# Kernel optimization log

Hardware: AMD Instinct MI355X
Metric: run time of the kernel (lower is better)

Reference implementation:

```python
import jax, jax.numpy as jnp
import numpy as np
import math

N_HEADS = 8

def setup_inputs() -> dict:
    key = jax.random.key(0)
    qkv = jax.random.normal(key, (4, 1536, 2048), dtype=jnp.float32)
    return {"qkv": qkv}

def reference(qkv) -> jnp.ndarray:
    bs, width, length = qkv.shape
    ch = width // (3 * N_HEADS)
    q, k, v = jnp.split(qkv, 3, axis=1)  # each (bs, n_heads*ch, T)
    scale = 1.0 / math.sqrt(math.sqrt(ch))
    q = (q * scale).reshape(bs * N_HEADS, ch, length)
    k = (k * scale).reshape(bs * N_HEADS, ch, length)
    v = v.reshape(bs * N_HEADS, ch, length)
    # scores: (bs*heads, T, T)
    weight = jnp.einsum('bct,bcs->bts', q, k)
    weight = jax.nn.softmax(weight.astype(jnp.float32), axis=-1).astype(weight.dtype)
    a = jnp.einsum('bts,bcs->bct', weight, v)
    return a.reshape(bs, -1, length)
```

## Files before the change

kernel.cpp:

```cpp
#include <hip/hip_runtime.h>
#include <hip/hip_bf16.h>
#include <math.h>


#define T_LEN 2048
#define NH    32
#define D     64
#define QLD   2048
#define LSTR  72

using f32x4 = __attribute__((ext_vector_type(4))) float;
using s16x8 = __attribute__((ext_vector_type(8))) short;
using s16x4 = __attribute__((ext_vector_type(4))) short;
using u32x4 = __attribute__((ext_vector_type(4))) unsigned;

__device__ __forceinline__ short f2bf(float f) {
    union { float f; unsigned u; } x; x.f = f;
    unsigned r = x.u + 0x7fffu + ((x.u >> 16) & 1u);
    return (short)(r >> 16);
}

#if __has_builtin(__builtin_amdgcn_exp2f)
#define EXP2(x) __builtin_amdgcn_exp2f(x)
#else
#define EXP2(x) __expf(0.6931471805599453f * (x))
#endif

__device__ __forceinline__ unsigned pack2bf(float a, float b) {
    unsigned ua = __float_as_uint(a) + 0x8000u;
    unsigned ub = __float_as_uint(b) + 0x8000u;
    return __builtin_amdgcn_perm(ub, ua, 0x07060302u);
}

__global__ __launch_bounds__(256, 4)
void prep(const float* __restrict__ qkv, short* __restrict__ ws16)
{
    __shared__ __align__(16) short tile[64 * LSTR];
    const int tid  = threadIdx.x;
    const int t0   = blockIdx.x * 64;
    const int head = blockIdx.y;
    const int kind = blockIdx.z;
    const int b = head >> 3, h = head & 7;

    short* qt = ws16;
    short* kt = ws16 + (size_t)NH * T_LEN * D;
    short* vb = kt   + (size_t)NH * T_LEN * D;

    if (kind == 2) {
        const float* src = qkv + (size_t)(b * 1536 + 1024 + h * 64) * QLD;
        int c = tid >> 2, seg = (tid & 3) * 16;
        const float* p = src + (size_t)c * QLD + t0 + seg;
        short* dst = vb + ((size_t)head * D + c) * T_LEN + t0 + seg;
        #pragma unroll
        for (int j = 0; j < 2; ++j) {
            f32x4 a  = *(const f32x4*)(p + j * 8);
            f32x4 bb = *(const f32x4*)(p + j * 8 + 4);
            s16x8 w;
            w[0]=f2bf(a[0]);  w[1]=f2bf(a[1]);  w[2]=f2bf(a[2]);  w[3]=f2bf(a[3]);
            w[4]=f2bf(bb[0]); w[5]=f2bf(bb[1]); w[6]=f2bf(bb[2]); w[7]=f2bf(bb[3]);
            *(s16x8*)(dst + j * 8) = w;
        }
        return;
    }

    const float sc = (kind == 0) ? 0.35355339059327373f * 1.4426950408889634f
                                 : 0.35355339059327373f;
    const float* src = qkv + (size_t)(b * 1536 + kind * 512 + h * 64) * QLD;
    short* dst = (kind == 0 ? qt : kt) + ((size_t)head * T_LEN + t0) * D;

    {
        int m = tid & 15, c4 = (tid >> 4) << 2;
        const float* base = src + (size_t)c4 * QLD + t0 + 4 * m;
        f32x4 r0 = *(const f32x4*)base;
        f32x4 r1 = *(const f32x4*)(base + QLD);
        f32x4 r2 = *(const f32x4*)(base + 2 * QLD);
        f32x4 r3 = *(const f32x4*)(base + 3 * QLD);
        #pragma unroll
        for (int j = 0; j < 4; ++j) {
            s16x4 w;
            w[0]=f2bf(r0[j]*sc); w[1]=f2bf(r1[j]*sc); w[2]=f2bf(r2[j]*sc); w[3]=f2bf(r3[j]*sc);
            *(s16x4*)&tile[(4 * m + j) * LSTR + c4] = w;
        }
    }
    __syncthreads();
    {
        int row = tid >> 3;
        int off = (tid & 7) * 8;
        *(s16x8*)(dst + (size_t)row * D + off)        = *(const s16x8*)&tile[row * LSTR + off];
        *(s16x8*)(dst + (size_t)(row + 32) * D + off) = *(const s16x8*)&tile[(row + 32) * LSTR + off];
    }
}

__global__ __launch_bounds__(256, 4)
void attn(const short* __restrict__ ws16, float* __restrict__ out)
{
    __shared__ __align__(16) short ktile[64 * 64];
    __shared__ __align__(16) short vtile[64 * 64];

    const int tid  = threadIdx.x;
    const int w    = tid >> 6;
    const int lane = tid & 63;
    const int l16  = lane & 15;
    const int quad = lane >> 4;

    const int bid  = blockIdx.x;
    const int head = (bid & 7) + 8 * ((bid >> 3) & 3);
    const int t0   = (bid >> 5) * 64;

    const short* qt = ws16 + (size_t)head * T_LEN * D;
    const short* kt = ws16 + (size_t)NH * T_LEN * D + (size_t)head * T_LEN * D;
    const short* vb = ws16 + 2 * (size_t)NH * T_LEN * D + (size_t)head * D * T_LEN;
    float*       op = out  + (size_t)head * 64 * QLD;

    const short* qrow = qt + (size_t)(t0 + w * 16 + l16) * D + quad * 8;
    const s16x8 bq0 = *(const s16x8*)qrow;
    const s16x8 bq1 = *(const s16x8*)(qrow + 32);

    f32x4 o[4];
    #pragma unroll
    for (int ct = 0; ct < 4; ++ct) o[ct] = f32x4{0.f, 0.f, 0.f, 0.f};
    float l_part = 0.f;

    const int kperm = (l16 >> 2) * 8 + (l16 & 3);
    const int ksw   = (l16 & 3) | (((l16 >> 2) & 1) << 2);
    const int srow  = lane >> 3;
    const int schk  = lane & 7;

    for (int it = 0; it < T_LEN / 64; ++it) {
        const int s0 = it * 64;

        #pragma unroll
        for (int n = 0; n < 2; ++n) {
            const int rl = w * 16 + n * 8 + srow;
            const int sk = (srow & 3) | (((w * 2 + n) & 1) << 2);
            s16x8 kd = *(const s16x8*)(kt + (size_t)(s0 + rl) * D + ((schk ^ sk) << 3));
            *(s16x8*)&ktile[rl * 64 + schk * 8] = kd;
            s16x8 vd = *(const s16x8*)(vb + (size_t)rl * T_LEN + s0 + ((schk ^ srow) << 3));
            *(s16x8*)&vtile[rl * 64 + schk * 8] = vd;
        }
        __syncthreads();

        #pragma unroll
        for (int g = 0; g < 2; ++g) {
            u32x4 bp;
            #pragma unroll
            for (int sub = 0; sub < 2; ++sub) {
                const int R = g * 32 + kperm + 4 * sub;
                const int c0 = (quad ^ ksw) << 3;
                s16x8 ak0 = *(const s16x8*)&ktile[R * 64 + c0];
                s16x8 ak1 = *(const s16x8*)&ktile[R * 64 + (c0 ^ 32)];
                f32x4 acc = f32x4{0.f, 0.f, 0.f, 0.f};
                acc = __builtin_amdgcn_mfma_f32_16x16x32_bf16(ak0, bq0, acc, 0, 0, 0);
                acc = __builtin_amdgcn_mfma_f32_16x16x32_bf16(ak1, bq1, acc, 0, 0, 0);
                float p0 = EXP2(acc[0]);
                float p1 = EXP2(acc[1]);
                float p2 = EXP2(acc[2]);
                float p3 = EXP2(acc[3]);
                l_part += (p0 + p1) + (p2 + p3);
                bp[sub * 2]     = pack2bf(p0, p1);
                bp[sub * 2 + 1] = pack2bf(p2, p3);
            }
            #pragma unroll
            for (int ct = 0; ct < 4; ++ct) {
                const int r = ct * 16 + l16;
                s16x8 av = *(const s16x8*)&vtile[r * 64 + ((((g * 4 + quad) ^ (l16 & 7))) << 3)];
                o[ct] = __builtin_amdgcn_mfma_f32_16x16x32_bf16(
                    av, __builtin_bit_cast(s16x8, bp), o[ct], 0, 0, 0);
            }
        }
        __syncthreads();
    }

    float l = l_part;
    l += __shfl_xor(l, 16);
    l += __shfl_xor(l, 32);
    const float inv = 1.f / l;
    const int tq = t0 + w * 16 + l16;
    #pragma unroll
    for (int ct = 0; ct < 4; ++ct) {
        #pragma unroll
        for (int r = 0; r < 4; ++r) {
            const int c = ct * 16 + quad * 4 + r;
            op[(size_t)c * QLD + tq] = o[ct][r] * inv;
        }
    }
}

extern "C" void kernel_launch(void* const* d_in, const int* in_sizes, int n_in,
                              void* d_out, int out_size, void* d_ws, size_t ws_size,
                              hipStream_t stream) {
    const float* qkv = (const float*)d_in[0];
    float* out = (float*)d_out;
    short* ws16 = (short*)d_ws;

    prep<<<dim3(T_LEN / 64, NH, 3), dim3(256), 0, stream>>>(qkv, ws16);
    attn<<<dim3(1024), dim3(256), 0, stream>>>(ws16, out);
}
```

Before: 135.5 us.

## Process two query sub-tiles per wave to reuse K/V tiles across 128 queries

Each block now handles 128 query rows instead of 64, with each wave computing two 16-row query sub-tiles that share the same K and V fragments loaded from LDS. This halves the global K/V traffic per query and the LDS reads per MFMA. In exchange it doubles accumulator registers, lowers occupancy (launch bounds reduced to 2), and halves the grid to 512 blocks, which may underfill the 256 CUs.

Measured after the change: 156.7 us. +15.7%, slower.

```diff
diff --git a/kernel.cpp b/kernel.cpp
--- a/kernel.cpp
+++ b/kernel.cpp
@@ -91,7 +91,7 @@
     }
 }
 
-__global__ __launch_bounds__(256, 4)
+__global__ __launch_bounds__(256, 2)
 void attn(const short* __restrict__ ws16, float* __restrict__ out)
 {
     __shared__ __align__(16) short ktile[64 * 64];
@@ -105,21 +105,27 @@
 
     const int bid  = blockIdx.x;
     const int head = (bid & 7) + 8 * ((bid >> 3) & 3);
-    const int t0   = (bid >> 5) * 64;
+    const int t0   = (bid >> 5) * 128;
 
     const short* qt = ws16 + (size_t)head * T_LEN * D;
     const short* kt = ws16 + (size_t)NH * T_LEN * D + (size_t)head * T_LEN * D;
     const short* vb = ws16 + 2 * (size_t)NH * T_LEN * D + (size_t)head * D * T_LEN;
     float*       op = out  + (size_t)head * 64 * QLD;
 
-    const short* qrow = qt + (size_t)(t0 + w * 16 + l16) * D + quad * 8;
-    const s16x8 bq0 = *(const s16x8*)qrow;
-    const s16x8 bq1 = *(const s16x8*)(qrow + 32);
-
-    f32x4 o[4];
+    s16x8 bq[2][2];
     #pragma unroll
-    for (int ct = 0; ct < 4; ++ct) o[ct] = f32x4{0.f, 0.f, 0.f, 0.f};
-    float l_part = 0.f;
+    for (int nq = 0; nq < 2; ++nq) {
+        const short* qrow = qt + (size_t)(t0 + w * 32 + nq * 16 + l16) * D + quad * 8;
+        bq[nq][0] = *(const s16x8*)qrow;
+        bq[nq][1] = *(const s16x8*)(qrow + 32);
+    }
+
+    f32x4 o[2][4];
+    #pragma unroll
+    for (int nq = 0; nq < 2; ++nq)
+        #pragma unroll
+        for (int ct = 0; ct < 4; ++ct) o[nq][ct] = f32x4{0.f, 0.f, 0.f, 0.f};
+    float l_part[2] = {0.f, 0.f};
 
     const int kperm = (l16 >> 2) * 8 + (l16 & 3);
     const int ksw   = (l16 & 3) | (((l16 >> 2) & 1) << 2);
@@ -142,46 +148,55 @@
 
         #pragma unroll
         for (int g = 0; g < 2; ++g) {
-            u32x4 bp;
+            u32x4 bp[2];
             #pragma unroll
             for (int sub = 0; sub < 2; ++sub) {
                 const int R = g * 32 + kperm + 4 * sub;
                 const int c0 = (quad ^ ksw) << 3;
                 s16x8 ak0 = *(const s16x8*)&ktile[R * 64 + c0];
                 s16x8 ak1 = *(const s16x8*)&ktile[R * 64 + (c0 ^ 32)];
-                f32x4 acc = f32x4{0.f, 0.f, 0.f, 0.f};
-                acc = __builtin_amdgcn_mfma_f32_16x16x32_bf16(ak0, bq0, acc, 0, 0, 0);
-                acc = __builtin_amdgcn_mfma_f32_16x16x32_bf16(ak1, bq1, acc, 0, 0, 0);
-                float p0 = EXP2(acc[0]);
-                float p1 = EXP2(acc[1]);
-                float p2 = EXP2(acc[2]);
-                float p3 = EXP2(acc[3]);
-                l_part += (p0 + p1) + (p2 + p3);
-                bp[sub * 2]     = pack2bf(p0, p1);
-                bp[sub * 2 + 1] = pack2bf(p2, p3);
+                #pragma unroll
+                for (int nq = 0; nq < 2; ++nq) {
+                    f32x4 acc = f32x4{0.f, 0.f, 0.f, 0.f};
+                    acc = __builtin_amdgcn_mfma_f32_16x16x32_bf16(ak0, bq[nq][0], acc, 0, 0, 0);
+                    acc = __builtin_amdgcn_mfma_f32_16x16x32_bf16(ak1, bq[nq][1], acc, 0, 0, 0);
+                    float p0 = EXP2(acc[0]);
+                    float p1 = EXP2(acc[1]);
+                    float p2 = EXP2(acc[2]);
+                    float p3 = EXP2(acc[3]);
+                    l_part[nq] += (p0 + p1) + (p2 + p3);
+                    bp[nq][sub * 2]     = pack2bf(p0, p1);
+                    bp[nq][sub * 2 + 1] = pack2bf(p2, p3);
+                }
             }
             #pragma unroll
             for (int ct = 0; ct < 4; ++ct) {
                 const int r = ct * 16 + l16;
                 s16x8 av = *(const s16x8*)&vtile[r * 64 + ((((g * 4 + quad) ^ (l16 & 7))) << 3)];
-                o[ct] = __builtin_amdgcn_mfma_f32_16x16x32_bf16(
-                    av, __builtin_bit_cast(s16x8, bp), o[ct], 0, 0, 0);
+                #pragma unroll
+                for (int nq = 0; nq < 2; ++nq) {
+                    o[nq][ct] = __builtin_amdgcn_mfma_f32_16x16x32_bf16(
+                        av, __builtin_bit_cast(s16x8, bp[nq]), o[nq][ct], 0, 0, 0);
+                }
             }
         }
         __syncthreads();
     }
 
-    float l = l_part;
-    l += __shfl_xor(l, 16);
-    l += __shfl_xor(l, 32);
-    const float inv = 1.f / l;
-    const int tq = t0 + w * 16 + l16;
     #pragma unroll
-    for (int ct = 0; ct < 4; ++ct) {
-        #pragma unroll
-        for (int r = 0; r < 4; ++r) {
-            const int c = ct * 16 + quad * 4 + r;
-            op[(size_t)c * QLD + tq] = o[ct][r] * inv;
+    for (int nq = 0; nq < 2; ++nq) {
+        float l = l_part[nq];
+        l += __shfl_xor(l, 16);
+        l += __shfl_xor(l, 32);
+        const float inv = 1.f / l;
+        const int tq = t0 + w * 32 + nq * 16 + l16;
+        #pragma unroll
+        for (int ct = 0; ct < 4; ++ct) {
+            #pragma unroll
+            for (int r = 0; r < 4; ++r) {
+                const int c = ct * 16 + quad * 4 + r;
+                op[(size_t)c * QLD + tq] = o[nq][ct][r] * inv;
+            }
         }
     }
 }
@@ -194,5 +209,5 @@
     short* ws16 = (short*)d_ws;
 
     prep<<<dim3(T_LEN / 64, NH, 3), dim3(256), 0, stream>>>(qkv, ws16);
-    attn<<<dim3(1024), dim3(256), 0, stream>>>(ws16, out);
-}
+    attn<<<dim3(512), dim3(256), 0, stream>>>(ws16, out);
+}
```

## Double-buffer K/V LDS tiles and prefetch next tile during compute

Applied to the files above, without the earlier changes.

Splits the K and V shared-memory tiles into two buffers. Global loads for the next iteration are issued before the MFMA work on the current tile and written to the other buffer afterwards, leaving one barrier per iteration instead of two. The aim is to hide global-memory latency behind the QK/PV compute. In exchange it doubles LDS use to 32KB per block, which could lower occupancy, and keeps the prefetched registers live across the compute.

Measured after the change: 134.7 us. Within noise of the previous version (-0.6%).

```diff
diff --git a/kernel.cpp b/kernel.cpp
--- a/kernel.cpp
+++ b/kernel.cpp
@@ -94,8 +94,8 @@
 __global__ __launch_bounds__(256, 4)
 void attn(const short* __restrict__ ws16, float* __restrict__ out)
 {
-    __shared__ __align__(16) short ktile[64 * 64];
-    __shared__ __align__(16) short vtile[64 * 64];
+    __shared__ __align__(16) short ktile[2][64 * 64];
+    __shared__ __align__(16) short vtile[2][64 * 64];
 
     const int tid  = threadIdx.x;
     const int w    = tid >> 6;
@@ -126,19 +126,36 @@
     const int srow  = lane >> 3;
     const int schk  = lane & 7;
 
+    const int rl0 = w * 16 + srow;
+    const int rl1 = rl0 + 8;
+    const int sk0 = (srow & 3) | (((w * 2 + 0) & 1) << 2);
+    const int sk1 = (srow & 3) | (((w * 2 + 1) & 1) << 2);
+    const short* kge0 = kt + (size_t)rl0 * D + ((schk ^ sk0) << 3);
+    const short* kge1 = kt + (size_t)rl1 * D + ((schk ^ sk1) << 3);
+    const short* vge0 = vb + (size_t)rl0 * T_LEN + ((schk ^ srow) << 3);
+    const short* vge1 = vb + (size_t)rl1 * T_LEN + ((schk ^ srow) << 3);
+
+    {
+        s16x8 kd0 = *(const s16x8*)(kge0);
+        s16x8 kd1 = *(const s16x8*)(kge1);
+        s16x8 vd0 = *(const s16x8*)(vge0);
+        s16x8 vd1 = *(const s16x8*)(vge1);
+        *(s16x8*)&ktile[0][rl0 * 64 + schk * 8] = kd0;
+        *(s16x8*)&ktile[0][rl1 * 64 + schk * 8] = kd1;
+        *(s16x8*)&vtile[0][rl0 * 64 + schk * 8] = vd0;
+        *(s16x8*)&vtile[0][rl1 * 64 + schk * 8] = vd1;
+    }
+
+    #pragma unroll 2
     for (int it = 0; it < T_LEN / 64; ++it) {
-        const int s0 = it * 64;
-
-        #pragma unroll
-        for (int n = 0; n < 2; ++n) {
-            const int rl = w * 16 + n * 8 + srow;
-            const int sk = (srow & 3) | (((w * 2 + n) & 1) << 2);
-            s16x8 kd = *(const s16x8*)(kt + (size_t)(s0 + rl) * D + ((schk ^ sk) << 3));
-            *(s16x8*)&ktile[rl * 64 + schk * 8] = kd;
-            s16x8 vd = *(const s16x8*)(vb + (size_t)rl * T_LEN + s0 + ((schk ^ srow) << 3));
-            *(s16x8*)&vtile[rl * 64 + schk * 8] = vd;
-        }
+        const int cur = it & 1;
         __syncthreads();
+
+        const int s0n = (it + 1 < T_LEN / 64 ? it + 1 : it) * 64;
+        s16x8 kd0 = *(const s16x8*)(kge0 + (size_t)s0n * D);
+        s16x8 kd1 = *(const s16x8*)(kge1 + (size_t)s0n * D);
+        s16x8 vd0 = *(const s16x8*)(vge0 + s0n);
+        s16x8 vd1 = *(const s16x8*)(vge1 + s0n);
 
         #pragma unroll
         for (int g = 0; g < 2; ++g) {
@@ -147,8 +164,8 @@
             for (int sub = 0; sub < 2; ++sub) {
                 const int R = g * 32 + kperm + 4 * sub;
                 const int c0 = (quad ^ ksw) << 3;
-                s16x8 ak0 = *(const s16x8*)&ktile[R * 64 + c0];
-                s16x8 ak1 = *(const s16x8*)&ktile[R * 64 + (c0 ^ 32)];
+                s16x8 ak0 = *(const s16x8*)&ktile[cur][R * 64 + c0];
+                s16x8 ak1 = *(const s16x8*)&ktile[cur][R * 64 + (c0 ^ 32)];
                 f32x4 acc = f32x4{0.f, 0.f, 0.f, 0.f};
                 acc = __builtin_amdgcn_mfma_f32_16x16x32_bf16(ak0, bq0, acc, 0, 0, 0);
                 acc = __builtin_amdgcn_mfma_f32_16x16x32_bf16(ak1, bq1, acc, 0, 0, 0);
@@ -163,12 +180,16 @@
             #pragma unroll
             for (int ct = 0; ct < 4; ++ct) {
                 const int r = ct * 16 + l16;
-                s16x8 av = *(const s16x8*)&vtile[r * 64 + ((((g * 4 + quad) ^ (l16 & 7))) << 3)];
+                s16x8 av = *(const s16x8*)&vtile[cur][r * 64 + ((((g * 4 + quad) ^ (l16 & 7))) << 3)];
                 o[ct] = __builtin_amdgcn_mfma_f32_16x16x32_bf16(
                     av, __builtin_bit_cast(s16x8, bp), o[ct], 0, 0, 0);
             }
         }
-        __syncthreads();
+
+        *(s16x8*)&ktile[cur ^ 1][rl0 * 64 + schk * 8] = kd0;
+        *(s16x8*)&ktile[cur ^ 1][rl1 * 64 + schk * 8] = kd1;
+        *(s16x8*)&vtile[cur ^ 1][rl0 * 64 + schk * 8] = vd0;
+        *(s16x8*)&vtile[cur ^ 1][rl1 * 64 + schk * 8] = vd1;
     }
 
     float l = l_part;
```
